# Kernel optimization log

Hardware: AMD Instinct MI355X
Metric: run time of the kernel (lower is better)

Reference implementation:

```python
import jax, jax.numpy as jnp
import numpy as np

N = 50000
E = 800000
DF = 8        # dim_feat
DH = 32       # dim_hidden = out_channels per head
H = 4         # heads
HC = H * DH
DE = 4        # edge_dim
DD = 256      # dim_dense
DO = 4        # dim_out
NL = 3        # num GAT layers
SLOPE = 0.2   # GAT negative_slope
NL_SLOPE = 0.01  # nn.LeakyReLU default


def setup_inputs() -> dict:
    key = jax.random.key(0)
    ks = jax.random.split(key, 32)
    p = lambda k, shp: (jax.random.normal(k, shp, dtype=jnp.float32) * 0.1)
    inp = {
        "x": jax.random.normal(ks[0], (N, DF), dtype=jnp.float32),
        "edge_index": jax.random.randint(ks[1], (2, E), 0, N, dtype=jnp.int64),
        "edge_attr": jax.random.normal(ks[2], (E, DE), dtype=jnp.float32),
        # layer 0 (in = DF)
        "Wl0": p(ks[3], (DF, HC)), "bl0": jnp.zeros((HC,), jnp.float32),
        "Wr0": p(ks[4], (DF, HC)), "br0": jnp.zeros((HC,), jnp.float32),
        "We0": p(ks[5], (DE, HC)),
        "att0": p(ks[6], (H, DH)),
        "bo0": jnp.zeros((DH,), jnp.float32),
        # layers 1..NL-1 stacked (in = DH)
        "Wl": p(ks[7], (NL - 1, DH, HC)), "bl": jnp.zeros((NL - 1, HC), jnp.float32),
        "Wr": p(ks[8], (NL - 1, DH, HC)), "br": jnp.zeros((NL - 1, HC), jnp.float32),
        "We": p(ks[9], (NL - 1, DE, HC)),
        "att": p(ks[10], (NL - 1, H, DH)),
        "bo": jnp.zeros((NL - 1, DH), jnp.float32),
        # MLP head
        "Wd1": p(ks[11], (DH, DD)), "bd1": jnp.zeros((DD,), jnp.float32),
        "Wd2": p(ks[12], (DD, DO)), "bd2": jnp.zeros((DO,), jnp.float32),
    }
    return inp


def gat_layer(x, src, dst, ea, Wl, bl, Wr, br, We, att, bo):
    # GATv2ConvNorm, concat=False, no self loops, eval (dropout off)
    xl = (x @ Wl + bl).reshape(-1, H, DH)   # source transform  [N,H,C]
    xr = (x @ Wr + br).reshape(-1, H, DH)   # target transform  [N,H,C]
    x_j = xl[src]                            # [E,H,C]
    x_i = xr[dst]                            # [E,H,C]
    ef = (ea @ We).reshape(-1, H, DH)        # [E,H,C]
    m = jax.nn.leaky_relu(x_i + x_j + ef, negative_slope=SLOPE)
    e = jnp.einsum('ehc,hc->eh', m, att)     # logits [E,H]
    # Lipschitz norm on logits
    ni = jnp.linalg.norm(x_i, axis=-1)       # [E,H]
    nj = jnp.linalg.norm(x_j, axis=-1)       # [E,H]
    mx = jax.ops.segment_max(nj, dst, num_segments=N)
    mx = jnp.where(jnp.isfinite(mx), mx, 0.0)  # empty groups -> 0 (torch include_self=False init)
    e = e / (4.0 * (ni + mx[dst]) + 1e-12)
    # scatter softmax over destination groups
    emax = jax.ops.segment_max(e, dst, num_segments=N)
    z = jnp.exp(e - emax[dst])
    s = jax.ops.segment_sum(z, dst, num_segments=N)
    alpha = z / (s[dst] + 1e-16)             # [E,H]
    out = jax.ops.segment_sum(alpha[..., None] * x_j, dst, num_segments=N)  # [N,H,C]
    return out.mean(axis=1) + bo             # concat=False -> mean over heads


def reference(x, edge_index, edge_attr, Wl0, bl0, Wr0, br0, We0, att0, bo0,
              Wl, bl, Wr, br, We, att, bo, Wd1, bd1, Wd2, bd2):
    src, dst = edge_index[0], edge_index[1]
    act = lambda a: jax.nn.leaky_relu(a, negative_slope=NL_SLOPE)
    h = act(gat_layer(x, src, dst, edge_attr, Wl0, bl0, Wr0, br0, We0, att0, bo0))
    for i in range(NL - 1):
        h = act(gat_layer(h, src, dst, edge_attr, Wl[i], bl[i], Wr[i], br[i], We[i], att[i], bo[i]))
    h = act(h @ Wd1 + bd1)
    return h @ Wd2 + bd2
```

## Files before the change

kernel.cpp:

```cpp
#include <hip/hip_runtime.h>
#include <hip/hip_fp16.h>
#include <math.h>

#define NN 50000
#define EE 800000
#define DFi 8
#define DHc 32
#define Hh 4
#define HCc 128
#define DEe 4
#define DDd 256
#define DOo 4

__global__ void detect_kernel(const unsigned int* __restrict__ w, int nwords, int* __restrict__ flag) {
    unsigned int acc = 0;
    for (int i = 2 * threadIdx.x + 1; i < nwords; i += 512) acc |= w[i];
    if (acc) atomicOr(flag, 1);
}

__global__ void convert_count_kernel(const void* __restrict__ buf, const int* __restrict__ flag,
                                     int* __restrict__ EI, int* __restrict__ counts) {
    int i = blockIdx.x * 256 + threadIdx.x;
    if (i >= 2 * EE) return;
    int v = (*flag) ? ((const int*)buf)[i] : (int)(((const long long*)buf)[i]);
    EI[i] = v;
    if (i >= EE) atomicAdd(&counts[v], 1);
}

__global__ void ea2h_kernel(const float4* __restrict__ EA4, __half* __restrict__ EAh) {
    int e = blockIdx.x * 256 + threadIdx.x;
    if (e >= EE) return;
    float4 a = EA4[e];
    __half2* o = reinterpret_cast<__half2*>(EAh + e * 4);
    o[0] = __floats2half2_rn(a.x, a.y);
    o[1] = __floats2half2_rn(a.z, a.w);
}

__global__ void scanA_kernel(const int* __restrict__ counts, int* __restrict__ roff,
                             int* __restrict__ bsum, int M) {
    __shared__ int sd[256];
    int t = threadIdx.x;
    int idx = blockIdx.x * 256 + t;
    int v = (idx < M) ? counts[idx] : 0;
    sd[t] = v;
    __syncthreads();
    for (int off = 1; off < 256; off <<= 1) {
        int x = (t >= off) ? sd[t - off] : 0;
        __syncthreads();
        sd[t] += x;
        __syncthreads();
    }
    if (idx < M) roff[idx] = sd[t] - v;
    if (t == 255) bsum[blockIdx.x] = sd[255];
}

__global__ void scanB_kernel(const int* __restrict__ bsum, int* __restrict__ boff, int nb) {
    __shared__ int sd[256];
    int t = threadIdx.x;
    int v = (t < nb) ? bsum[t] : 0;
    sd[t] = v;
    __syncthreads();
    for (int off = 1; off < 256; off <<= 1) {
        int x = (t >= off) ? sd[t - off] : 0;
        __syncthreads();
        sd[t] += x;
        __syncthreads();
    }
    boff[t] = sd[t] - v;
}

__global__ void scanC_kernel(int* __restrict__ roff, const int* __restrict__ boff, int M) {
    int idx = blockIdx.x * 256 + threadIdx.x;
    if (idx < M) roff[idx] += boff[idx >> 8];
}

__global__ void fill_kernel(const int* __restrict__ EI, const int* __restrict__ roff,
                            int* __restrict__ cursor, long long* __restrict__ ce) {
    int e = blockIdx.x * 256 + threadIdx.x;
    if (e >= EE) return;
    int d = EI[EE + e];
    int s = EI[e];
    int pos = atomicAdd(&cursor[d], 1);
    ce[roff[d] + pos] = ((long long)e << 32) | (unsigned int)s;
}

__global__ __launch_bounds__(256) void sortw_kernel(const int* __restrict__ roff,
                                                    long long* __restrict__ ce) {
    const int n = blockIdx.x * 4 + (threadIdx.x >> 6);
    if (n >= NN) return;
    const int lane = threadIdx.x & 63;
    const int a = roff[n];
    const int d = roff[n + 1] - a;
    if (d <= 1) return;
    if (d <= 64) {
        long long key = (lane < d) ? ce[a + lane] : 0x7fffffffffffffffLL;
#pragma unroll
        for (int k = 2; k <= 64; k <<= 1) {
#pragma unroll
            for (int j = k >> 1; j > 0; j >>= 1) {
                long long o = __shfl_xor(key, j);
                bool up = ((lane & k) == 0);
                bool lower = ((lane & j) == 0);
                long long mn = (o < key) ? o : key;
                long long mx = (o < key) ? key : o;
                key = (lower == up) ? mn : mx;
            }
        }
        if (lane < d) ce[a + lane] = key;
    } else if (lane == 0) {
        for (int i2 = a + 1; i2 < a + d; i2++) {
            long long kk = ce[i2];
            int j2 = i2 - 1;
            while (j2 >= a && ce[j2] > kk) { ce[j2 + 1] = ce[j2]; j2--; }
            ce[j2 + 1] = kk;
        }
    }
}

template <int IN>
__global__ __launch_bounds__(128) void transform_kernel(
    const float* __restrict__ Xin, const float* __restrict__ Wl, const float* __restrict__ bl,
    const float* __restrict__ Wr, const float* __restrict__ br,
    __half* __restrict__ XLh, float* __restrict__ XR,
    float* __restrict__ NLn, float* __restrict__ NRn) {
    const int t = threadIdx.x;
    float wl[IN], wr[IN];
#pragma unroll
    for (int k = 0; k < IN; k++) { wl[k] = Wl[k * HCc + t]; wr[k] = Wr[k * HCc + t]; }
    const float blv = bl[t], brv = br[t];
    __shared__ float xst[16][IN];
    const int nbeg = blockIdx.x * 16;
    for (int idx = t; idx < 16 * IN; idx += 128) {
        int r = idx / IN, cc = idx % IN;
        int n = nbeg + r;
        xst[r][cc] = (n < NN) ? Xin[n * IN + cc] : 0.f;
    }
    __syncthreads();
#pragma unroll 4
    for (int r = 0; r < 16; ++r) {
        int n = nbeg + r;
        if (n >= NN) break;
        float al = blv, ar = brv;
#pragma unroll
        for (int k = 0; k < IN; k++) { float xv = xst[r][k]; al = fmaf(xv, wl[k], al); ar = fmaf(xv, wr[k], ar); }
        XLh[n * HCc + t] = __float2half(al);
        XR[n * HCc + t] = ar;
        float sl = al * al, sr = ar * ar;
#pragma unroll
        for (int msk = 1; msk < 32; msk <<= 1) { sl += __shfl_xor(sl, msk); sr += __shfl_xor(sr, msk); }
        if ((t & 31) == 0) { NLn[n * 4 + (t >> 5)] = sqrtf(sl); NRn[n * 4 + (t >> 5)] = sqrtf(sr); }
    }
}

__device__ inline float4 h8tof4(uint2 r) {
    __half2 p0 = *reinterpret_cast<const __half2*>(&r.x);
    __half2 p1 = *reinterpret_cast<const __half2*>(&r.y);
    float2 lo = __half22float2(p0), hi = __half22float2(p1);
    return make_float4(lo.x, lo.y, hi.x, hi.y);
}

__global__ __launch_bounds__(256) void gat_kernel(
    const __half* __restrict__ XLh, const float* __restrict__ XR,
    const float* __restrict__ NLn, const float* __restrict__ NRn,
    const int* __restrict__ roff, const long long* __restrict__ ce,
    const __half* __restrict__ EAh, const float* __restrict__ We,
    const float* __restrict__ att, const float* __restrict__ bo,
    float* __restrict__ Hout) {
    const int lane = threadIdx.x & 63;
    const int wslot = blockIdx.x * 4 + (threadIdx.x >> 6);
    const int NW = gridDim.x * 4;
    const int c = lane & 31;
    const int g = lane >> 5;
    const int h = c >> 3;

    const uint2*  XLu2 = reinterpret_cast<const uint2*>(XLh);
    const uint2*  EAu2 = reinterpret_cast<const uint2*>(EAh);
    const float4* XR4 = reinterpret_cast<const float4*>(XR);
    const float4* NL4 = reinterpret_cast<const float4*>(NLn);
    const float4* We4 = reinterpret_cast<const float4*>(We);
    const float4* at4 = reinterpret_cast<const float4*>(att);
    const float4* bo4 = reinterpret_cast<const float4*>(bo);
    float4* Ho4 = reinterpret_cast<float4*>(Hout);

    const float4 w0 = We4[c], w1 = We4[32 + c], w2 = We4[64 + c], w3 = We4[96 + c];
    const float4 at = at4[c];

    for (int i = wslot; i < NN; i += NW) {
        const int base = roff[i];
        const int deg = roff[i + 1] - base;

        if (deg == 0) {
            if (lane < 8) {
                float4 b = bo4[lane];
                float4 r;
                r.x = b.x > 0.f ? b.x : 0.01f * b.x;
                r.y = b.y > 0.f ? b.y : 0.01f * b.y;
                r.z = b.z > 0.f ? b.z : 0.01f * b.z;
                r.w = b.w > 0.f ? b.w : 0.01f * b.w;
                Ho4[i * 8 + lane] = r;
            }
            continue;
        }

        const float4 xi = XR4[i * 32 + c];
        float srun = 0.f;
        float4 acc = make_float4(0.f, 0.f, 0.f, 0.f);
        float invD;

#define BODY(XR_, ER_, K)                                                         \
        {                                                                         \
            float4 xj = h8tof4(XR_);                                              \
            float4 a4 = h8tof4(ER_);                                              \
            float e0 = a4.x * w0.x; e0 = fmaf(a4.y, w1.x, e0);                    \
            e0 = fmaf(a4.z, w2.x, e0); e0 = fmaf(a4.w, w3.x, e0);                 \
            float e1 = a4.x * w0.y; e1 = fmaf(a4.y, w1.y, e1);                    \
            e1 = fmaf(a4.z, w2.y, e1); e1 = fmaf(a4.w, w3.y, e1);                 \
            float e2 = a4.x * w0.z; e2 = fmaf(a4.y, w1.z, e2);                    \
            e2 = fmaf(a4.z, w2.z, e2); e2 = fmaf(a4.w, w3.z, e2);                 \
            float e3 = a4.x * w0.w; e3 = fmaf(a4.y, w1.w, e3);                    \
            e3 = fmaf(a4.z, w2.w, e3); e3 = fmaf(a4.w, w3.w, e3);                 \
            float s0 = xi.x + xj.x + e0; s0 = s0 > 0.f ? s0 : 0.2f * s0;          \
            float s1 = xi.y + xj.y + e1; s1 = s1 > 0.f ? s1 : 0.2f * s1;          \
            float s2 = xi.z + xj.z + e2; s2 = s2 > 0.f ? s2 : 0.2f * s2;          \
            float s3 = xi.w + xj.w + e3; s3 = s3 > 0.f ? s3 : 0.2f * s3;          \
            float pp = s0 * at.x; pp = fmaf(s1, at.y, pp);                        \
            pp = fmaf(s2, at.z, pp); pp = fmaf(s3, at.w, pp);                     \
            pp += __shfl_xor(pp, 1); pp += __shfl_xor(pp, 2);                     \
            pp += __shfl_xor(pp, 4);                                              \
            float z = __expf(fminf(pp * invD, 60.f));                             \
            z = ((K) < deg) ? z : 0.f;                                            \
            srun += z;                                                            \
            acc.x = fmaf(z, xj.x, acc.x);                                         \
            acc.y = fmaf(z, xj.y, acc.y);                                         \
            acc.z = fmaf(z, xj.z, acc.z);                                         \
            acc.w = fmaf(z, xj.w, acc.w);                                         \
        }

        if (deg <= 64) {
            int jreg = 0, ereg = 0;
            if (lane < deg) {
                long long v = ce[base + lane];
                jreg = (int)(v & 0xffffffffLL);
                ereg = (int)(v >> 32);
            }
#define ISSUE(XR_, ER_, K)                                                        \
            {                                                                     \
                int kc = ((K) < deg) ? (K) : 0;                                   \
                int jx = __shfl(jreg, kc);                                        \
                int ex = __shfl(ereg, kc);                                        \
                XR_ = XLu2[jx * 32 + c];                                          \
                ER_ = EAu2[ex];                                                   \
            }
            uint2 xA, eA, xB, eB, xC, eC, xD, eD;
            ISSUE(xA, eA, g);
            ISSUE(xB, eB, g + 2);
            ISSUE(xC, eC, g + 4);
            ISSUE(xD, eD, g + 6);

            float4 mx = make_float4(0.f, 0.f, 0.f, 0.f);
            if (lane < deg) mx = NL4[jreg];
#pragma unroll
            for (int msk = 1; msk < 64; msk <<= 1) {
                mx.x = fmaxf(mx.x, __shfl_xor(mx.x, msk));
                mx.y = fmaxf(mx.y, __shfl_xor(mx.y, msk));
                mx.z = fmaxf(mx.z, __shfl_xor(mx.z, msk));
                mx.w = fmaxf(mx.w, __shfl_xor(mx.w, msk));
            }
            float mxh = (h == 0) ? mx.x : (h == 1) ? mx.y : (h == 2) ? mx.z : mx.w;
            invD = 1.0f / (4.0f * (NRn[i * 4 + h] + mxh) + 1e-12f);

            const int nsteps = (deg + 1) >> 1;
            for (int s = 0; s < nsteps; s += 4) {
                uint2 xE, eE, xF, eF, xG, eG, xH, eH;
                ISSUE(xE, eE, g + 2 * (s + 4));
                ISSUE(xF, eF, g + 2 * (s + 5));
                ISSUE(xG, eG, g + 2 * (s + 6));
                ISSUE(xH, eH, g + 2 * (s + 7));
                BODY(xA, eA, g + 2 * s);
                if (s + 1 < nsteps) BODY(xB, eB, g + 2 * (s + 1));
                if (s + 2 < nsteps) BODY(xC, eC, g + 2 * (s + 2));
                if (s + 3 < nsteps) BODY(xD, eD, g + 2 * (s + 3));
                xA = xE; eA = eE; xB = xF; eB = eF;
                xC = xG; eC = eG; xD = xH; eD = eH;
            }
#undef ISSUE
        } else {
            float4 mx = make_float4(0.f, 0.f, 0.f, 0.f);
            for (int k = lane; k < deg; k += 64) {
                long long v = ce[base + k];
                int j = (int)(v & 0xffffffffLL);
                float4 nj = NL4[j];
                mx.x = fmaxf(mx.x, nj.x); mx.y = fmaxf(mx.y, nj.y);
                mx.z = fmaxf(mx.z, nj.z); mx.w = fmaxf(mx.w, nj.w);
            }
#pragma unroll
            for (int msk = 1; msk < 64; msk <<= 1) {
                mx.x = fmaxf(mx.x, __shfl_xor(mx.x, msk));
                mx.y = fmaxf(mx.y, __shfl_xor(mx.y, msk));
                mx.z = fmaxf(mx.z, __shfl_xor(mx.z, msk));
                mx.w = fmaxf(mx.w, __shfl_xor(mx.w, msk));
            }
            float mxh = (h == 0) ? mx.x : (h == 1) ? mx.y : (h == 2) ? mx.z : mx.w;
            invD = 1.0f / (4.0f * (NRn[i * 4 + h] + mxh) + 1e-12f);

            for (int kk = g; kk < deg; kk += 2) {
                long long v = ce[base + kk];
                int jc = (int)(v & 0xffffffffLL);
                int ec = (int)(v >> 32);
                uint2 xr = XLu2[jc * 32 + c];
                uint2 er = EAu2[ec];
                BODY(xr, er, kk);
            }
        }
#undef BODY

        srun += __shfl_xor(srun, 32);
        acc.x += __shfl_xor(acc.x, 32);
        acc.y += __shfl_xor(acc.y, 32);
        acc.z += __shfl_xor(acc.z, 32);
        acc.w += __shfl_xor(acc.w, 32);
        float inv = 1.0f / (srun + 1e-16f);
        float a0 = acc.x * inv, a1 = acc.y * inv, a2 = acc.z * inv, a3 = acc.w * inv;
        a0 += __shfl_xor(a0, 8); a0 += __shfl_xor(a0, 16);
        a1 += __shfl_xor(a1, 8); a1 += __shfl_xor(a1, 16);
        a2 += __shfl_xor(a2, 8); a2 += __shfl_xor(a2, 16);
        a3 += __shfl_xor(a3, 8); a3 += __shfl_xor(a3, 16);

        if (lane < 8) {
            float4 b = bo4[lane];
            float4 r;
            r.x = fmaf(0.25f, a0, b.x); r.x = r.x > 0.f ? r.x : 0.01f * r.x;
            r.y = fmaf(0.25f, a1, b.y); r.y = r.y > 0.f ? r.y : 0.01f * r.y;
            r.z = fmaf(0.25f, a2, b.z); r.z = r.z > 0.f ? r.z : 0.01f * r.z;
            r.w = fmaf(0.25f, a3, b.w); r.w = r.w > 0.f ? r.w : 0.01f * r.w;
            Ho4[i * 8 + lane] = r;
        }
    }
}

__global__ __launch_bounds__(256) void mlp_kernel(
    const float* __restrict__ Hin, const float* __restrict__ Wd1, const float* __restrict__ bd1,
    const float* __restrict__ Wd2, const float* __restrict__ bd2, float* __restrict__ out) {
    const int lane = threadIdx.x & 63;
    const int chunk = __builtin_amdgcn_readfirstlane(threadIdx.x >> 6);
    const int nb = blockIdx.x * 64;
    int node = nb + lane;
    int nclamp = node < NN ? node : NN - 1;

    float h[32];
    const float4* H4 = reinterpret_cast<const float4*>(Hin);
#pragma unroll
    for (int r = 0; r < 8; ++r) {
        float4 t = H4[nclamp * 8 + r];
        h[4 * r] = t.x; h[4 * r + 1] = t.y; h[4 * r + 2] = t.z; h[4 * r + 3] = t.w;
    }

    float o0 = 0.f, o1 = 0.f, o2 = 0.f, o3 = 0.f;
    const int dbase = chunk * 64;
    for (int t = 0; t < 4; ++t) {
        float acc[16];
#pragma unroll
        for (int j = 0; j < 16; ++j) acc[j] = bd1[dbase + t * 16 + j];
#pragma unroll 8
        for (int k = 0; k < 32; ++k) {
            const float* wr = Wd1 + k * DDd + dbase + t * 16;
#pragma unroll
            for (int j = 0; j < 16; ++j) acc[j] = fmaf(h[k], wr[j], acc[j]);
        }
#pragma unroll
        for (int j = 0; j < 16; ++j) {
            float hd = acc[j];
            hd = hd > 0.f ? hd : 0.01f * hd;
            int d = dbase + t * 16 + j;
            o0 = fmaf(hd, Wd2[d * 4 + 0], o0);
            o1 = fmaf(hd, Wd2[d * 4 + 1], o1);
            o2 = fmaf(hd, Wd2[d * 4 + 2], o2);
            o3 = fmaf(hd, Wd2[d * 4 + 3], o3);
        }
    }

    __shared__ float4 red[4][64];
    red[chunk][lane] = make_float4(o0, o1, o2, o3);
    __syncthreads();
    if (threadIdx.x < 64 && nb + (int)threadIdx.x < NN) {
        float4 r0 = red[0][threadIdx.x], r1 = red[1][threadIdx.x];
        float4 r2 = red[2][threadIdx.x], r3 = red[3][threadIdx.x];
        float4 o;
        o.x = r0.x + r1.x + r2.x + r3.x + bd2[0];
        o.y = r0.y + r1.y + r2.y + r3.y + bd2[1];
        o.z = r0.z + r1.z + r2.z + r3.z + bd2[2];
        o.w = r0.w + r1.w + r2.w + r3.w + bd2[3];
        reinterpret_cast<float4*>(out)[nb + threadIdx.x] = o;
    }
}

extern "C" void kernel_launch(void* const* d_in, const int* in_sizes, int n_in,
                              void* d_out, int out_size, void* d_ws, size_t ws_size,
                              hipStream_t stream) {
    const float* x    = (const float*)d_in[0];
    const void*  eraw = d_in[1];
    const float* ea   = (const float*)d_in[2];
    const float* Wl0  = (const float*)d_in[3];
    const float* bl0  = (const float*)d_in[4];
    const float* Wr0  = (const float*)d_in[5];
    const float* br0  = (const float*)d_in[6];
    const float* We0  = (const float*)d_in[7];
    const float* att0 = (const float*)d_in[8];
    const float* bo0  = (const float*)d_in[9];
    const float* Wl   = (const float*)d_in[10];
    const float* bl   = (const float*)d_in[11];
    const float* Wr   = (const float*)d_in[12];
    const float* br   = (const float*)d_in[13];
    const float* We   = (const float*)d_in[14];
    const float* att  = (const float*)d_in[15];
    const float* bo   = (const float*)d_in[16];
    const float* Wd1  = (const float*)d_in[17];
    const float* bd1  = (const float*)d_in[18];
    const float* Wd2  = (const float*)d_in[19];
    const float* bd2  = (const float*)d_in[20];
    float* out = (float*)d_out;

    char* p = (char*)d_ws;
    auto alloc = [&](size_t bytes) { void* r = (void*)p; p += (bytes + 255) & ~(size_t)255; return r; };
    int*       EI     = (int*)alloc((size_t)2 * EE * 4);
    int*       counts = (int*)alloc((size_t)(NN + 1) * 4);
    int*       roff   = (int*)alloc((size_t)(NN + 1) * 4);
    int*       bsum   = (int*)alloc(256 * 4);
    int*       boff   = (int*)alloc(256 * 4);
    int*       cursor = (int*)alloc((size_t)NN * 4);
    long long* ce     = (long long*)alloc((size_t)EE * 8);
    int*       flag   = (int*)alloc(256);
    __half*    XLh    = (__half*)alloc((size_t)NN * HCc * 2);
    __half*    EAh    = (__half*)alloc((size_t)EE * 4 * 2);
    float*     XRb    = (float*)alloc((size_t)NN * HCc * 4);
    float*     NLn    = (float*)alloc((size_t)NN * 4 * 4);
    float*     NRn    = (float*)alloc((size_t)NN * 4 * 4);
    float*     HA     = (float*)alloc((size_t)NN * DHc * 4);
    float*     HB     = (float*)alloc((size_t)NN * DHc * 4);

    (void)hipMemsetAsync(counts, 0, (size_t)(NN + 1) * 4, stream);
    (void)hipMemsetAsync(cursor, 0, (size_t)NN * 4, stream);
    (void)hipMemsetAsync(flag, 0, 4, stream);

    detect_kernel<<<1, 256, 0, stream>>>((const unsigned int*)eraw, 8192, flag);
    convert_count_kernel<<<(2 * EE + 255) / 256, 256, 0, stream>>>(eraw, flag, EI, counts);
    ea2h_kernel<<<(EE + 255) / 256, 256, 0, stream>>>((const float4*)ea, EAh);
    const int M = NN + 1;
    const int NBLK = (M + 255) / 256;
    scanA_kernel<<<NBLK, 256, 0, stream>>>(counts, roff, bsum, M);
    scanB_kernel<<<1, 256, 0, stream>>>(bsum, boff, NBLK);
    scanC_kernel<<<NBLK, 256, 0, stream>>>(roff, boff, M);
    fill_kernel<<<(EE + 255) / 256, 256, 0, stream>>>(EI, roff, cursor, ce);
    sortw_kernel<<<(NN + 3) / 4, 256, 0, stream>>>(roff, ce);

    const int gT = (NN + 15) / 16;
    const int gG = 2048;

    transform_kernel<DFi><<<gT, 128, 0, stream>>>(x, Wl0, bl0, Wr0, br0, XLh, XRb, NLn, NRn);
    gat_kernel<<<gG, 256, 0, stream>>>(XLh, XRb, NLn, NRn, roff, ce, EAh, We0, att0, bo0, HA);
    transform_kernel<DHc><<<gT, 128, 0, stream>>>(HA, Wl, bl, Wr, br, XLh, XRb, NLn, NRn);
    gat_kernel<<<gG, 256, 0, stream>>>(XLh, XRb, NLn, NRn, roff, ce, EAh, We, att, bo, HB);
    transform_kernel<DHc><<<gT, 128, 0, stream>>>(HB, Wl + DHc * HCc, bl + HCc, Wr + DHc * HCc, br + HCc,
                                                  XLh, XRb, NLn, NRn);
    gat_kernel<<<gG, 256, 0, stream>>>(XLh, XRb, NLn, NRn, roff, ce, EAh, We + DEe * HCc,
                                       att + Hh * DHc, bo + DHc, HA);
    mlp_kernel<<<(NN + 63) / 64, 256, 0, stream>>>(HA, Wd1, bd1, Wd2, bd2, out);
}
```

Before: 491.2 us.

## Process four edges per wave with 8 channels per lane in GAT aggregation

Each lane of the GAT aggregation kernel now handles 8 feature channels, loaded as a 16-byte fp16 vector, instead of 4. A 64-lane wave therefore processes four neighbour edges at once instead of two. The software prefetch pipeline is reshaped from four to three outstanding edge groups, and the final reductions are adjusted to combine four edge groups and the heads. This aims to halve the per-edge steps for low-degree nodes and issue wider gathers, at the cost of more registers and more lanes idle on small-degree nodes.

```diff
diff --git a/kernel.cpp b/kernel.cpp
--- a/kernel.cpp
+++ b/kernel.cpp
@@ -152,9 +152,9 @@
     }
 }
 
-__device__ inline float4 h8tof4(uint2 r) {
-    __half2 p0 = *reinterpret_cast<const __half2*>(&r.x);
-    __half2 p1 = *reinterpret_cast<const __half2*>(&r.y);
+__device__ inline float4 h8tof4(unsigned int a, unsigned int b) {
+    __half2 p0 = *reinterpret_cast<const __half2*>(&a);
+    __half2 p1 = *reinterpret_cast<const __half2*>(&b);
     float2 lo = __half22float2(p0), hi = __half22float2(p1);
     return make_float4(lo.x, lo.y, hi.x, hi.y);
 }
@@ -169,11 +169,11 @@
     const int lane = threadIdx.x & 63;
     const int wslot = blockIdx.x * 4 + (threadIdx.x >> 6);
     const int NW = gridDim.x * 4;
-    const int c = lane & 31;
-    const int g = lane >> 5;
-    const int h = c >> 3;
-
-    const uint2*  XLu2 = reinterpret_cast<const uint2*>(XLh);
+    const int c = lane & 15;
+    const int g = lane >> 4;
+    const int h = c >> 2;
+
+    const uint4*  XLu4 = reinterpret_cast<const uint4*>(XLh);
     const uint2*  EAu2 = reinterpret_cast<const uint2*>(EAh);
     const float4* XR4 = reinterpret_cast<const float4*>(XR);
     const float4* NL4 = reinterpret_cast<const float4*>(NLn);
@@ -182,8 +182,11 @@
     const float4* bo4 = reinterpret_cast<const float4*>(bo);
     float4* Ho4 = reinterpret_cast<float4*>(Hout);
 
-    const float4 w0 = We4[c], w1 = We4[32 + c], w2 = We4[64 + c], w3 = We4[96 + c];
-    const float4 at = at4[c];
+    const float4 w0l = We4[2 * c],      w0h = We4[2 * c + 1];
+    const float4 w1l = We4[32 + 2 * c], w1h = We4[32 + 2 * c + 1];
+    const float4 w2l = We4[64 + 2 * c], w2h = We4[64 + 2 * c + 1];
+    const float4 w3l = We4[96 + 2 * c], w3h = We4[96 + 2 * c + 1];
+    const float4 atl = at4[2 * c],      ath = at4[2 * c + 1];
 
     for (int i = wslot; i < NN; i += NW) {
         const int base = roff[i];
@@ -202,38 +205,57 @@
             continue;
         }
 
-        const float4 xi = XR4[i * 32 + c];
+        const float4 xil = XR4[i * 32 + 2 * c], xih = XR4[i * 32 + 2 * c + 1];
         float srun = 0.f;
-        float4 acc = make_float4(0.f, 0.f, 0.f, 0.f);
+        float4 accl = make_float4(0.f, 0.f, 0.f, 0.f);
+        float4 acch = make_float4(0.f, 0.f, 0.f, 0.f);
         float invD;
 
-#define BODY(XR_, ER_, K)                                                         \
+#define BODY(X_, E_, K)                                                           \
         {                                                                         \
-            float4 xj = h8tof4(XR_);                                              \
-            float4 a4 = h8tof4(ER_);                                              \
-            float e0 = a4.x * w0.x; e0 = fmaf(a4.y, w1.x, e0);                    \
-            e0 = fmaf(a4.z, w2.x, e0); e0 = fmaf(a4.w, w3.x, e0);                 \
-            float e1 = a4.x * w0.y; e1 = fmaf(a4.y, w1.y, e1);                    \
-            e1 = fmaf(a4.z, w2.y, e1); e1 = fmaf(a4.w, w3.y, e1);                 \
-            float e2 = a4.x * w0.z; e2 = fmaf(a4.y, w1.z, e2);                    \
-            e2 = fmaf(a4.z, w2.z, e2); e2 = fmaf(a4.w, w3.z, e2);                 \
-            float e3 = a4.x * w0.w; e3 = fmaf(a4.y, w1.w, e3);                    \
-            e3 = fmaf(a4.z, w2.w, e3); e3 = fmaf(a4.w, w3.w, e3);                 \
-            float s0 = xi.x + xj.x + e0; s0 = s0 > 0.f ? s0 : 0.2f * s0;          \
-            float s1 = xi.y + xj.y + e1; s1 = s1 > 0.f ? s1 : 0.2f * s1;          \
-            float s2 = xi.z + xj.z + e2; s2 = s2 > 0.f ? s2 : 0.2f * s2;          \
-            float s3 = xi.w + xj.w + e3; s3 = s3 > 0.f ? s3 : 0.2f * s3;          \
-            float pp = s0 * at.x; pp = fmaf(s1, at.y, pp);                        \
-            pp = fmaf(s2, at.z, pp); pp = fmaf(s3, at.w, pp);                     \
+            float4 xjl = h8tof4((X_).x, (X_).y);                                  \
+            float4 xjh = h8tof4((X_).z, (X_).w);                                  \
+            float4 a4 = h8tof4((E_).x, (E_).y);                                   \
+            float e0 = a4.x * w0l.x; e0 = fmaf(a4.y, w1l.x, e0);                  \
+            e0 = fmaf(a4.z, w2l.x, e0); e0 = fmaf(a4.w, w3l.x, e0);               \
+            float e1 = a4.x * w0l.y; e1 = fmaf(a4.y, w1l.y, e1);                  \
+            e1 = fmaf(a4.z, w2l.y, e1); e1 = fmaf(a4.w, w3l.y, e1);               \
+            float e2 = a4.x * w0l.z; e2 = fmaf(a4.y, w1l.z, e2);                  \
+            e2 = fmaf(a4.z, w2l.z, e2); e2 = fmaf(a4.w, w3l.z, e2);               \
+            float e3 = a4.x * w0l.w; e3 = fmaf(a4.y, w1l.w, e3);                  \
+            e3 = fmaf(a4.z, w2l.w, e3); e3 = fmaf(a4.w, w3l.w, e3);               \
+            float e4 = a4.x * w0h.x; e4 = fmaf(a4.y, w1h.x, e4);                  \
+            e4 = fmaf(a4.z, w2h.x, e4); e4 = fmaf(a4.w, w3h.x, e4);               \
+            float e5 = a4.x * w0h.y; e5 = fmaf(a4.y, w1h.y, e5);                  \
+            e5 = fmaf(a4.z, w2h.y, e5); e5 = fmaf(a4.w, w3h.y, e5);               \
+            float e6 = a4.x * w0h.z; e6 = fmaf(a4.y, w1h.z, e6);                  \
+            e6 = fmaf(a4.z, w2h.z, e6); e6 = fmaf(a4.w, w3h.z, e6);               \
+            float e7 = a4.x * w0h.w; e7 = fmaf(a4.y, w1h.w, e7);                  \
+            e7 = fmaf(a4.z, w2h.w, e7); e7 = fmaf(a4.w, w3h.w, e7);               \
+            float s0 = xil.x + xjl.x + e0; s0 = s0 > 0.f ? s0 : 0.2f * s0;        \
+            float s1 = xil.y + xjl.y + e1; s1 = s1 > 0.f ? s1 : 0.2f * s1;        \
+            float s2 = xil.z + xjl.z + e2; s2 = s2 > 0.f ? s2 : 0.2f * s2;        \
+            float s3 = xil.w + xjl.w + e3; s3 = s3 > 0.f ? s3 : 0.2f * s3;        \
+            float s4 = xih.x + xjh.x + e4; s4 = s4 > 0.f ? s4 : 0.2f * s4;        \
+            float s5 = xih.y + xjh.y + e5; s5 = s5 > 0.f ? s5 : 0.2f * s5;        \
+            float s6 = xih.z + xjh.z + e6; s6 = s6 > 0.f ? s6 : 0.2f * s6;        \
+            float s7 = xih.w + xjh.w + e7; s7 = s7 > 0.f ? s7 : 0.2f * s7;        \
+            float pp = s0 * atl.x; pp = fmaf(s1, atl.y, pp);                      \
+            pp = fmaf(s2, atl.z, pp); pp = fmaf(s3, atl.w, pp);                   \
+            pp = fmaf(s4, ath.x, pp); pp = fmaf(s5, ath.y, pp);                   \
+            pp = fmaf(s6, ath.z, pp); pp = fmaf(s7, ath.w, pp);                   \
             pp += __shfl_xor(pp, 1); pp += __shfl_xor(pp, 2);                     \
-            pp += __shfl_xor(pp, 4);                                              \
             float z = __expf(fminf(pp * invD, 60.f));                             \
             z = ((K) < deg) ? z : 0.f;                                            \
             srun += z;                                                            \
-            acc.x = fmaf(z, xj.x, acc.x);                                         \
-            acc.y = fmaf(z, xj.y, acc.y);                                         \
-            acc.z = fmaf(z, xj.z, acc.z);                                         \
-            acc.w = fmaf(z, xj.w, acc.w);                                         \
+            accl.x = fmaf(z, xjl.x, accl.x);                                      \
+            accl.y = fmaf(z, xjl.y, accl.y);                                      \
+            accl.z = fmaf(z, xjl.z, accl.z);                                      \
+            accl.w = fmaf(z, xjl.w, accl.w);                                      \
+            acch.x = fmaf(z, xjh.x, acch.x);                                      \
+            acch.y = fmaf(z, xjh.y, acch.y);                                      \
+            acch.z = fmaf(z, xjh.z, acch.z);                                      \
+            acch.w = fmaf(z, xjh.w, acch.w);                                      \
         }
 
         if (deg <= 64) {
@@ -243,19 +265,19 @@
                 jreg = (int)(v & 0xffffffffLL);
                 ereg = (int)(v >> 32);
             }
-#define ISSUE(XR_, ER_, K)                                                        \
+#define ISSUE(X_, E_, K)                                                          \
             {                                                                     \
                 int kc = ((K) < deg) ? (K) : 0;                                   \
                 int jx = __shfl(jreg, kc);                                        \
                 int ex = __shfl(ereg, kc);                                        \
-                XR_ = XLu2[jx * 32 + c];                                          \
-                ER_ = EAu2[ex];                                                   \
-            }
-            uint2 xA, eA, xB, eB, xC, eC, xD, eD;
+                X_ = XLu4[jx * 16 + c];                                           \
+                E_ = EAu2[ex];                                                    \
+            }
+            uint4 xA, xB, xC;
+            uint2 eA, eB, eC;
             ISSUE(xA, eA, g);
-            ISSUE(xB, eB, g + 2);
-            ISSUE(xC, eC, g + 4);
-            ISSUE(xD, eD, g + 6);
+            ISSUE(xB, eB, 4 + g);
+            ISSUE(xC, eC, 8 + g);
 
             float4 mx = make_float4(0.f, 0.f, 0.f, 0.f);
             if (lane < deg) mx = NL4[jreg];
@@ -269,19 +291,17 @@
             float mxh = (h == 0) ? mx.x : (h == 1) ? mx.y : (h == 2) ? mx.z : mx.w;
             invD = 1.0f / (4.0f * (NRn[i * 4 + h] + mxh) + 1e-12f);
 
-            const int nsteps = (deg + 1) >> 1;
-            for (int s = 0; s < nsteps; s += 4) {
-                uint2 xE, eE, xF, eF, xG, eG, xH, eH;
-                ISSUE(xE, eE, g + 2 * (s + 4));
-                ISSUE(xF, eF, g + 2 * (s + 5));
-                ISSUE(xG, eG, g + 2 * (s + 6));
-                ISSUE(xH, eH, g + 2 * (s + 7));
-                BODY(xA, eA, g + 2 * s);
-                if (s + 1 < nsteps) BODY(xB, eB, g + 2 * (s + 1));
-                if (s + 2 < nsteps) BODY(xC, eC, g + 2 * (s + 2));
-                if (s + 3 < nsteps) BODY(xD, eD, g + 2 * (s + 3));
-                xA = xE; eA = eE; xB = xF; eB = eF;
-                xC = xG; eC = eG; xD = xH; eD = eH;
+            const int nsteps = (deg + 3) >> 2;
+            for (int s = 0; s < nsteps; s += 3) {
+                uint4 xD, xE, xF;
+                uint2 eD, eE, eF;
+                ISSUE(xD, eD, 4 * (s + 3) + g);
+                ISSUE(xE, eE, 4 * (s + 4) + g);
+                ISSUE(xF, eF, 4 * (s + 5) + g);
+                BODY(xA, eA, 4 * s + g);
+                if (s + 1 < nsteps) BODY(xB, eB, 4 * (s + 1) + g);
+                if (s + 2 < nsteps) BODY(xC, eC, 4 * (s + 2) + g);
+                xA = xD; eA = eD; xB = xE; eB = eE; xC = xF; eC = eF;
             }
 #undef ISSUE
         } else {
@@ -303,37 +323,51 @@
             float mxh = (h == 0) ? mx.x : (h == 1) ? mx.y : (h == 2) ? mx.z : mx.w;
             invD = 1.0f / (4.0f * (NRn[i * 4 + h] + mxh) + 1e-12f);
 
-            for (int kk = g; kk < deg; kk += 2) {
+            for (int kk = g; kk < deg; kk += 4) {
                 long long v = ce[base + kk];
                 int jc = (int)(v & 0xffffffffLL);
                 int ec = (int)(v >> 32);
-                uint2 xr = XLu2[jc * 32 + c];
+                uint4 xr = XLu4[jc * 16 + c];
                 uint2 er = EAu2[ec];
                 BODY(xr, er, kk);
             }
         }
 #undef BODY
 
-        srun += __shfl_xor(srun, 32);
-        acc.x += __shfl_xor(acc.x, 32);
-        acc.y += __shfl_xor(acc.y, 32);
-        acc.z += __shfl_xor(acc.z, 32);
-        acc.w += __shfl_xor(acc.w, 32);
+        srun += __shfl_xor(srun, 16); srun += __shfl_xor(srun, 32);
+        accl.x += __shfl_xor(accl.x, 16); accl.x += __shfl_xor(accl.x, 32);
+        accl.y += __shfl_xor(accl.y, 16); accl.y += __shfl_xor(accl.y, 32);
+        accl.z += __shfl_xor(accl.z, 16); accl.z += __shfl_xor(accl.z, 32);
+        accl.w += __shfl_xor(accl.w, 16); accl.w += __shfl_xor(accl.w, 32);
+        acch.x += __shfl_xor(acch.x, 16); acch.x += __shfl_xor(acch.x, 32);
+        acch.y += __shfl_xor(acch.y, 16); acch.y += __shfl_xor(acch.y, 32);
+        acch.z += __shfl_xor(acch.z, 16); acch.z += __shfl_xor(acch.z, 32);
+        acch.w += __shfl_xor(acch.w, 16); acch.w += __shfl_xor(acch.w, 32);
         float inv = 1.0f / (srun + 1e-16f);
-        float a0 = acc.x * inv, a1 = acc.y * inv, a2 = acc.z * inv, a3 = acc.w * inv;
-        a0 += __shfl_xor(a0, 8); a0 += __shfl_xor(a0, 16);
-        a1 += __shfl_xor(a1, 8); a1 += __shfl_xor(a1, 16);
-        a2 += __shfl_xor(a2, 8); a2 += __shfl_xor(a2, 16);
-        a3 += __shfl_xor(a3, 8); a3 += __shfl_xor(a3, 16);
-
-        if (lane < 8) {
-            float4 b = bo4[lane];
-            float4 r;
-            r.x = fmaf(0.25f, a0, b.x); r.x = r.x > 0.f ? r.x : 0.01f * r.x;
-            r.y = fmaf(0.25f, a1, b.y); r.y = r.y > 0.f ? r.y : 0.01f * r.y;
-            r.z = fmaf(0.25f, a2, b.z); r.z = r.z > 0.f ? r.z : 0.01f * r.z;
-            r.w = fmaf(0.25f, a3, b.w); r.w = r.w > 0.f ? r.w : 0.01f * r.w;
-            Ho4[i * 8 + lane] = r;
+        float a0 = accl.x * inv, a1 = accl.y * inv, a2 = accl.z * inv, a3 = accl.w * inv;
+        float a4_ = acch.x * inv, a5 = acch.y * inv, a6 = acch.z * inv, a7 = acch.w * inv;
+        a0 += __shfl_xor(a0, 4); a0 += __shfl_xor(a0, 8);
+        a1 += __shfl_xor(a1, 4); a1 += __shfl_xor(a1, 8);
+        a2 += __shfl_xor(a2, 4); a2 += __shfl_xor(a2, 8);
+        a3 += __shfl_xor(a3, 4); a3 += __shfl_xor(a3, 8);
+        a4_ += __shfl_xor(a4_, 4); a4_ += __shfl_xor(a4_, 8);
+        a5 += __shfl_xor(a5, 4); a5 += __shfl_xor(a5, 8);
+        a6 += __shfl_xor(a6, 4); a6 += __shfl_xor(a6, 8);
+        a7 += __shfl_xor(a7, 4); a7 += __shfl_xor(a7, 8);
+
+        if (lane < 4) {
+            float4 bl_ = bo4[2 * lane], bh_ = bo4[2 * lane + 1];
+            float4 rl, rh;
+            rl.x = fmaf(0.25f, a0, bl_.x); rl.x = rl.x > 0.f ? rl.x : 0.01f * rl.x;
+            rl.y = fmaf(0.25f, a1, bl_.y); rl.y = rl.y > 0.f ? rl.y : 0.01f * rl.y;
+            rl.z = fmaf(0.25f, a2, bl_.z); rl.z = rl.z > 0.f ? rl.z : 0.01f * rl.z;
+            rl.w = fmaf(0.25f, a3, bl_.w); rl.w = rl.w > 0.f ? rl.w : 0.01f * rl.w;
+            rh.x = fmaf(0.25f, a4_, bh_.x); rh.x = rh.x > 0.f ? rh.x : 0.01f * rh.x;
+            rh.y = fmaf(0.25f, a5, bh_.y); rh.y = rh.y > 0.f ? rh.y : 0.01f * rh.y;
+            rh.z = fmaf(0.25f, a6, bh_.z); rh.z = rh.z > 0.f ? rh.z : 0.01f * rh.z;
+            rh.w = fmaf(0.25f, a7, bh_.w); rh.w = rh.w > 0.f ? rh.w : 0.01f * rh.w;
+            Ho4[i * 8 + 2 * lane] = rl;
+            Ho4[i * 8 + 2 * lane + 1] = rh;
         }
     }
 }
```

Result: no change. 496.3 us (+1.0%).
